# Kernel optimization log

Measured on AMD Instinct MI355X. Metric: run time of the kernel, lower is better.

## Reference

```python
import jax, jax.numpy as jnp
import numpy as np

B, L, DI = 256, 64, 2048   # batch, image regions, image feature dim
T, DT = 32, 512            # caption length, text embedding dim
U, A = 512, 512            # GRU units, attention units


def setup_inputs() -> dict:
    key = jax.random.key(0)
    ks = jax.random.split(key, 14)
    s = 0.02
    return {
        "img": jax.random.normal(ks[0], (B, L, DI), jnp.float32),
        "text": jax.random.normal(ks[1], (B, T, DT), jnp.float32),
        "kernel": jax.random.normal(ks[2], (DI + DT, 3 * U), jnp.float32) * s,
        "input_bias": jax.random.normal(ks[3], (3 * U,), jnp.float32) * s,
        "recurrent_kernel": jax.random.normal(ks[4], (U, 3 * U), jnp.float32) * s,
        "recurrent_bias": jax.random.normal(ks[5], (3 * U,), jnp.float32) * s,
        "att_img_kernel": jax.random.normal(ks[6], (DI, A), jnp.float32) * s,
        "att_img_bias": jax.random.normal(ks[7], (A,), jnp.float32) * s,
        "att_hidden_kernel": jax.random.normal(ks[8], (U, A), jnp.float32) * s,
        "att_hidden_bias": jax.random.normal(ks[9], (A,), jnp.float32) * s,
        "att_v_kernel": jax.random.normal(ks[10], (A, 1), jnp.float32) * s,
        "att_v_bias": jax.random.normal(ks[11], (1,), jnp.float32) * s,
    }


def reference(img, text, kernel, input_bias, recurrent_kernel, recurrent_bias,
              att_img_kernel, att_img_bias, att_hidden_kernel, att_hidden_bias,
              att_v_kernel, att_v_bias):
    # Precompute the image attention projection (independent of h; the
    # original recomputes it each step, but the math is identical).
    img_proj = jnp.einsum('bld,da->bla', img, att_img_kernel) + att_img_bias  # [B,L,A]

    def step(h, x_t):
        # Bahdanau attention over image regions
        hid = jnp.tanh(img_proj + (h @ att_hidden_kernel + att_hidden_bias)[:, None, :])  # [B,L,A]
        score = hid @ att_v_kernel + att_v_bias                # [B,L,1]
        attw = jax.nn.softmax(score, axis=1)                   # softmax over regions
        ctx = jnp.sum(attw * img, axis=1)                      # [B,DI]
        # GRU gate math (keras GRU v2 convention, reset gate applied after matmul)
        inp = jnp.concatenate([x_t, ctx], axis=-1)             # [B,DT+DI]
        mx = inp @ kernel + input_bias                         # [B,3U]
        mi = h @ recurrent_kernel + recurrent_bias             # [B,3U]
        x_z, x_r, x_h = jnp.split(mx, 3, axis=-1)
        r_z, r_r, r_h = jnp.split(mi, 3, axis=-1)
        z = jax.nn.sigmoid(x_z + r_z)
        r = jax.nn.sigmoid(x_r + r_r)
        hh = jnp.tanh(x_h + r * r_h)
        h_new = z * h + (1.0 - z) * hh
        return h_new, h_new

    h0 = jnp.zeros((img.shape[0], recurrent_kernel.shape[0]), img.dtype)
    _, seq = jax.lax.scan(step, h0, jnp.swapaxes(text, 0, 1))  # seq: [T,B,U]
    return jnp.swapaxes(seq, 0, 1)                             # [B,T,U]
```

## Files before the change

kernel.cpp:

```cpp
#include <hip/hip_runtime.h>
#include <hip/hip_bf16.h>

#define B_  256
#define L_  64
#define DI_ 2048
#define T_  32
#define DT_ 512
#define U_  512
#define A_  512
#define N3U 1536

typedef short short8 __attribute__((ext_vector_type(8)));
typedef float floatx4 __attribute__((ext_vector_type(4)));

__device__ __forceinline__ unsigned short f2bf(float f) {
  unsigned int u = __float_as_uint(f);
  u += 0x7fffu + ((u >> 16) & 1u);
  return (unsigned short)(u >> 16);
}
__device__ __forceinline__ float bf2f(unsigned short s) {
  return __uint_as_float(((unsigned int)s) << 16);
}
__device__ __forceinline__ float fast_tanh(float x) {
  x = fminf(fmaxf(x, -15.f), 15.f);
  float e = __expf(2.f * x);
  return (e - 1.f) / (e + 1.f);
}

__global__ __launch_bounds__(256) void gemm_a32_bt16_mfma(
    const float* __restrict__ A, const unsigned short* __restrict__ Bt,
    const float* __restrict__ bias, void* __restrict__ Cout,
    int M, int N, int K, int out_bf16) {
  __shared__ unsigned short As[128][40];
  __shared__ unsigned short Bs[128][40];
  const int tid  = threadIdx.x;
  const int wave = tid >> 6;
  const int lane = tid & 63;
  const int quad = lane >> 4;
  const int lr   = lane & 15;
  const int wrow = (wave >> 1) * 64;
  const int wcol = (wave & 1) * 64;
  const size_t bm = (size_t)blockIdx.y * 128;
  const size_t bn = (size_t)blockIdx.x * 128;

  const int sr = tid >> 2;
  const int sc = (tid & 3) * 8;

  floatx4 acc[4][4] = {};

  for (int k0 = 0; k0 < K; k0 += 32) {
#pragma unroll
    for (int it = 0; it < 2; ++it) {
      const int row = sr + it * 64;
      const float* ap = A + (bm + row) * (size_t)K + k0 + sc;
      float4 a0 = *(const float4*)(ap);
      float4 a1 = *(const float4*)(ap + 4);
      short8 pk;
      pk[0] = (short)f2bf(a0.x); pk[1] = (short)f2bf(a0.y);
      pk[2] = (short)f2bf(a0.z); pk[3] = (short)f2bf(a0.w);
      pk[4] = (short)f2bf(a1.x); pk[5] = (short)f2bf(a1.y);
      pk[6] = (short)f2bf(a1.z); pk[7] = (short)f2bf(a1.w);
      *(short8*)&As[row][sc] = pk;
      *(float4*)&Bs[row][sc] = *(const float4*)(Bt + (bn + row) * (size_t)K + k0 + sc);
    }
    __syncthreads();
    short8 af[4], bf[4];
#pragma unroll
    for (int mi = 0; mi < 4; ++mi) af[mi] = *(const short8*)&As[wrow + mi * 16 + lr][quad * 8];
#pragma unroll
    for (int ni = 0; ni < 4; ++ni) bf[ni] = *(const short8*)&Bs[wcol + ni * 16 + lr][quad * 8];
#pragma unroll
    for (int mi = 0; mi < 4; ++mi)
#pragma unroll
      for (int ni = 0; ni < 4; ++ni)
        acc[mi][ni] = __builtin_amdgcn_mfma_f32_16x16x32_bf16(af[mi], bf[ni], acc[mi][ni], 0, 0, 0);
    __syncthreads();
  }

  float* outf = (float*)Cout;
  unsigned short* outb = (unsigned short*)Cout;
#pragma unroll
  for (int mi = 0; mi < 4; ++mi) {
#pragma unroll
    for (int ni = 0; ni < 4; ++ni) {
      const size_t row0 = bm + wrow + mi * 16 + quad * 4;
      const size_t col  = bn + wcol + ni * 16 + lr;
      const float bsum = bias ? bias[col] : 0.f;
#pragma unroll
      for (int reg = 0; reg < 4; ++reg) {
        const float v = acc[mi][ni][reg] + bsum;
        if (out_bf16) outb[(row0 + reg) * (size_t)N + col] = f2bf(v);
        else          outf[(row0 + reg) * (size_t)N + col] = v;
      }
    }
  }
}

__global__ void zero_f32(float* __restrict__ p, int n) {
  int i = blockIdx.x * 256 + threadIdx.x;
  if (i < n) p[i] = 0.f;
}

__global__ __launch_bounds__(256) void transpose_f32_bf16(
    const float* __restrict__ in, unsigned short* __restrict__ outp, int K, int N) {
  __shared__ unsigned short tile[32][33];
  const int tid = threadIdx.x;
  const int tx = tid & 31, ty = tid >> 5;
  const int k0 = blockIdx.y * 32, n0 = blockIdx.x * 32;
#pragma unroll
  for (int i = 0; i < 4; ++i) {
    const int kk = ty + i * 8;
    tile[tx][kk] = f2bf(in[(size_t)(k0 + kk) * N + n0 + tx]);
  }
  __syncthreads();
#pragma unroll
  for (int i = 0; i < 4; ++i) {
    const int nn = ty + i * 8;
    outp[(size_t)(n0 + nn) * K + k0 + tx] = tile[nn][tx];
  }
}

__global__ void build_bcat(const float* __restrict__ ahb,
                           const float* __restrict__ rb,
                           float* __restrict__ bcat) {
  int i = blockIdx.x * 256 + threadIdx.x;
  if (i < A_) bcat[i] = ahb[i];
  else if (i < A_ + N3U) bcat[i] = rb[i - A_];
}

__global__ __launch_bounds__(512) void attn_gru_step(
    const unsigned short* __restrict__ img_proj,
    const unsigned short* __restrict__ imgW,
    const float* __restrict__ text_proj,
    const float* __restrict__ hm,
    const float* __restrict__ vk,
    float* __restrict__ h,
    float* __restrict__ out,
    int t) {
  const int b = blockIdx.x;
  const int tid = threadIdx.x;
  const int lane = tid & 63;
  const int wave = tid >> 6;
  __shared__ float sc[L_];
  __shared__ float aw[L_];

  const float* hpg = hm + (size_t)b * 2048;
  float hpv[8], vvv[8];
  {
    float4 h0 = *(const float4*)(hpg + lane * 8);
    float4 h1 = *(const float4*)(hpg + lane * 8 + 4);
    float4 v0 = *(const float4*)(vk + lane * 8);
    float4 v1 = *(const float4*)(vk + lane * 8 + 4);
    hpv[0]=h0.x; hpv[1]=h0.y; hpv[2]=h0.z; hpv[3]=h0.w;
    hpv[4]=h1.x; hpv[5]=h1.y; hpv[6]=h1.z; hpv[7]=h1.w;
    vvv[0]=v0.x; vvv[1]=v0.y; vvv[2]=v0.z; vvv[3]=v0.w;
    vvv[4]=v1.x; vvv[5]=v1.y; vvv[6]=v1.z; vvv[7]=v1.w;
  }

#pragma unroll
  for (int i = 0; i < 8; ++i) {
    const int l = wave + i * 8;
    const unsigned short* ip = img_proj + ((size_t)b * L_ + l) * A_ + lane * 8;
    short8 v8 = *(const short8*)ip;
    float s = 0.f;
#pragma unroll
    for (int j = 0; j < 8; ++j) {
      s += fast_tanh(bf2f((unsigned short)v8[j]) + hpv[j]) * vvv[j];
    }
#pragma unroll
    for (int off = 32; off; off >>= 1) s += __shfl_down(s, off);
    if (lane == 0) sc[l] = s;
  }
  __syncthreads();

  if (tid < 64) {
    float x = sc[tid];
    float m = x;
#pragma unroll
    for (int off = 32; off; off >>= 1) m = fmaxf(m, __shfl_xor(m, off));
    float e = __expf(x - m);
    float ssum = e;
#pragma unroll
    for (int off = 32; off; off >>= 1) ssum += __shfl_xor(ssum, off);
    aw[tid] = e / ssum;
  }
  __syncthreads();

  const int u = tid;
  const unsigned short* iw = imgW + (size_t)b * L_ * N3U + u;
  float s0 = 0.f, s1 = 0.f, s2 = 0.f;
#pragma unroll 8
  for (int l = 0; l < L_; ++l) {
    const float a = aw[l];
    const unsigned short* p = iw + l * N3U;
    s0 += a * bf2f(p[0]);
    s1 += a * bf2f(p[512]);
    s2 += a * bf2f(p[1024]);
  }
  const float* tp  = text_proj + ((size_t)b * T_ + t) * N3U;
  const float* mib = hm + (size_t)b * 2048 + 512;
  const float xz = s0 + tp[u]        + mib[u];
  const float xr = s1 + tp[512 + u]  + mib[512 + u];
  const float xh = s2 + tp[1024 + u];
  const float rh = mib[1024 + u];
  const float z = 1.f / (1.f + __expf(-xz));
  const float r = 1.f / (1.f + __expf(-xr));
  const float hh = fast_tanh(xh + r * rh);
  const float hn = z * h[b * U_ + u] + (1.f - z) * hh;
  h[b * U_ + u] = hn;
  out[((size_t)b * T_ + t) * U_ + u] = hn;
}

extern "C" void kernel_launch(void* const* d_in, const int* in_sizes, int n_in,
                              void* d_out, int out_size, void* d_ws, size_t ws_size,
                              hipStream_t stream) {
  const float* img        = (const float*)d_in[0];
  const float* text       = (const float*)d_in[1];
  const float* kern       = (const float*)d_in[2];
  const float* input_bias = (const float*)d_in[3];
  const float* rec_kern   = (const float*)d_in[4];
  const float* rec_bias   = (const float*)d_in[5];
  const float* att_img_k  = (const float*)d_in[6];
  const float* att_img_b  = (const float*)d_in[7];
  const float* att_hid_k  = (const float*)d_in[8];
  const float* att_hid_b  = (const float*)d_in[9];
  const float* att_v_k    = (const float*)d_in[10];
  float* out = (float*)d_out;

  char* ws = (char*)d_ws;
  size_t off = 0;
  auto alloc = [&](size_t bytes) { char* p = ws + off; off += (bytes + 255) & ~(size_t)255; return p; };
  unsigned short* img_proj = (unsigned short*)alloc((size_t)B_*L_*A_*2);
  unsigned short* imgW     = (unsigned short*)alloc((size_t)B_*L_*N3U*2);
  float*          text_proj= (float*)         alloc((size_t)B_*T_*N3U*4);
  unsigned short* wt1      = (unsigned short*)alloc((size_t)A_*DI_*2);
  unsigned short* wt2      = (unsigned short*)alloc((size_t)N3U*DI_*2);
  unsigned short* wt3      = (unsigned short*)alloc((size_t)N3U*DT_*2);
  unsigned short* wcatT    = (unsigned short*)alloc((size_t)2048*U_*2);
  float*          bcat     = (float*)         alloc(2048*4);
  float*          h        = (float*)         alloc((size_t)B_*U_*4);
  float*          hm       = (float*)         alloc((size_t)B_*2048*4);

  dim3 blk(256);

  zero_f32<<<dim3((B_*U_ + 255) / 256), blk, 0, stream>>>(h, B_*U_);

  transpose_f32_bf16<<<dim3(A_/32, DI_/32), blk, 0, stream>>>(att_img_k, wt1, DI_, A_);
  transpose_f32_bf16<<<dim3(N3U/32, DI_/32), blk, 0, stream>>>(kern + (size_t)DT_*N3U, wt2, DI_, N3U);
  transpose_f32_bf16<<<dim3(N3U/32, DT_/32), blk, 0, stream>>>(kern, wt3, DT_, N3U);
  transpose_f32_bf16<<<dim3(A_/32, U_/32), blk, 0, stream>>>(att_hid_k, wcatT, U_, A_);
  transpose_f32_bf16<<<dim3(N3U/32, U_/32), blk, 0, stream>>>(rec_kern, wcatT + (size_t)A_*U_, U_, N3U);
  build_bcat<<<dim3(8), blk, 0, stream>>>(att_hid_b, rec_bias, bcat);

  gemm_a32_bt16_mfma<<<dim3(A_/128, (B_*L_)/128), blk, 0, stream>>>(
      img, wt1, att_img_b, img_proj, B_*L_, A_, DI_, 1);
  gemm_a32_bt16_mfma<<<dim3(N3U/128, (B_*L_)/128), blk, 0, stream>>>(
      img, wt2, nullptr, imgW, B_*L_, N3U, DI_, 1);
  gemm_a32_bt16_mfma<<<dim3(N3U/128, (B_*T_)/128), blk, 0, stream>>>(
      text, wt3, input_bias, text_proj, B_*T_, N3U, DT_, 0);

  for (int t = 0; t < T_; ++t) {
    gemm_a32_bt16_mfma<<<dim3(2048/128, B_/128), blk, 0, stream>>>(
        h, wcatT, bcat, hm, B_, 2048, U_, 0);
    attn_gru_step<<<dim3(B_), dim3(512), 0, stream>>>(
        img_proj, imgW, text_proj, hm, att_v_k, h, out, t);
  }
}
```

Measured before the change: 1.765 ms.

## Fuse recurrent loop into single cooperative kernel with grid syncs

Result: slower. 3.473 ms (+96.7%).

```diff
diff --git a/kernel.cpp b/kernel.cpp
--- a/kernel.cpp
+++ b/kernel.cpp
@@ -1,5 +1,8 @@
 #include <hip/hip_runtime.h>
 #include <hip/hip_bf16.h>
+#include <hip/hip_cooperative_groups.h>
+
+namespace cg = cooperative_groups;
 
 #define B_  256
 #define L_  64
@@ -25,6 +28,9 @@
   x = fminf(fmaxf(x, -15.f), 15.f);
   float e = __expf(2.f * x);
   return (e - 1.f) / (e + 1.f);
+}
+__device__ __forceinline__ float sigmoidf(float x) {
+  return 1.f / (1.f + __expf(-x));
 }
 
 __global__ __launch_bounds__(256) void gemm_a32_bt16_mfma(
@@ -96,11 +102,6 @@
   }
 }
 
-__global__ void zero_f32(float* __restrict__ p, int n) {
-  int i = blockIdx.x * 256 + threadIdx.x;
-  if (i < n) p[i] = 0.f;
-}
-
 __global__ __launch_bounds__(256) void transpose_f32_bf16(
     const float* __restrict__ in, unsigned short* __restrict__ outp, int K, int N) {
   __shared__ unsigned short tile[32][33];
@@ -128,87 +129,130 @@
   else if (i < A_ + N3U) bcat[i] = rb[i - A_];
 }
 
-__global__ __launch_bounds__(512) void attn_gru_step(
+__global__ __launch_bounds__(512) void recurrence_coop(
     const unsigned short* __restrict__ img_proj,
     const unsigned short* __restrict__ imgW,
     const float* __restrict__ text_proj,
-    const float* __restrict__ hm,
+    const unsigned short* __restrict__ wcatT,
+    const float* __restrict__ bcat,
     const float* __restrict__ vk,
     float* __restrict__ h,
-    float* __restrict__ out,
-    int t) {
-  const int b = blockIdx.x;
-  const int tid = threadIdx.x;
+    unsigned short* __restrict__ hbf,
+    float* __restrict__ hm,
+    float* __restrict__ out) {
+  cg::grid_group grid = cg::this_grid();
+  const int bid  = blockIdx.x;
+  const int tid  = threadIdx.x;
   const int lane = tid & 63;
   const int wave = tid >> 6;
+  const int quad = lane >> 4;
+  const int lr   = lane & 15;
+
   __shared__ float sc[L_];
   __shared__ float aw[L_];
-
-  const float* hpg = hm + (size_t)b * 2048;
-  float hpv[8], vvv[8];
+  __shared__ float mxs[N3U];
+
+  h[bid * U_ + tid] = 0.f;
+  hbf[bid * U_ + tid] = 0;
+  grid.sync();
+
+  const int n0  = (bid >> 1) * 16;
+  const int m0w = (bid & 1) * 128 + wave * 16;
+  const float bsum = bcat[n0 + lr];
+
+  float vvv[8];
   {
-    float4 h0 = *(const float4*)(hpg + lane * 8);
-    float4 h1 = *(const float4*)(hpg + lane * 8 + 4);
     float4 v0 = *(const float4*)(vk + lane * 8);
     float4 v1 = *(const float4*)(vk + lane * 8 + 4);
-    hpv[0]=h0.x; hpv[1]=h0.y; hpv[2]=h0.z; hpv[3]=h0.w;
-    hpv[4]=h1.x; hpv[5]=h1.y; hpv[6]=h1.z; hpv[7]=h1.w;
     vvv[0]=v0.x; vvv[1]=v0.y; vvv[2]=v0.z; vvv[3]=v0.w;
     vvv[4]=v1.x; vvv[5]=v1.y; vvv[6]=v1.z; vvv[7]=v1.w;
   }
 
-#pragma unroll
-  for (int i = 0; i < 8; ++i) {
-    const int l = wave + i * 8;
-    const unsigned short* ip = img_proj + ((size_t)b * L_ + l) * A_ + lane * 8;
-    short8 v8 = *(const short8*)ip;
-    float s = 0.f;
-#pragma unroll
-    for (int j = 0; j < 8; ++j) {
-      s += fast_tanh(bf2f((unsigned short)v8[j]) + hpv[j]) * vvv[j];
-    }
-#pragma unroll
-    for (int off = 32; off; off >>= 1) s += __shfl_down(s, off);
-    if (lane == 0) sc[l] = s;
-  }
-  __syncthreads();
-
-  if (tid < 64) {
-    float x = sc[tid];
-    float m = x;
-#pragma unroll
-    for (int off = 32; off; off >>= 1) m = fmaxf(m, __shfl_xor(m, off));
-    float e = __expf(x - m);
-    float ssum = e;
-#pragma unroll
-    for (int off = 32; off; off >>= 1) ssum += __shfl_xor(ssum, off);
-    aw[tid] = e / ssum;
-  }
-  __syncthreads();
-
-  const int u = tid;
-  const unsigned short* iw = imgW + (size_t)b * L_ * N3U + u;
-  float s0 = 0.f, s1 = 0.f, s2 = 0.f;
-#pragma unroll 8
-  for (int l = 0; l < L_; ++l) {
-    const float a = aw[l];
-    const unsigned short* p = iw + l * N3U;
-    s0 += a * bf2f(p[0]);
-    s1 += a * bf2f(p[512]);
-    s2 += a * bf2f(p[1024]);
-  }
-  const float* tp  = text_proj + ((size_t)b * T_ + t) * N3U;
-  const float* mib = hm + (size_t)b * 2048 + 512;
-  const float xz = s0 + tp[u]        + mib[u];
-  const float xr = s1 + tp[512 + u]  + mib[512 + u];
-  const float xh = s2 + tp[1024 + u];
-  const float rh = mib[1024 + u];
-  const float z = 1.f / (1.f + __expf(-xz));
-  const float r = 1.f / (1.f + __expf(-xr));
-  const float hh = fast_tanh(xh + r * rh);
-  const float hn = z * h[b * U_ + u] + (1.f - z) * hh;
-  h[b * U_ + u] = hn;
-  out[((size_t)b * T_ + t) * U_ + u] = hn;
+  for (int t = 0; t < T_; ++t) {
+    {
+      floatx4 acc = {0.f, 0.f, 0.f, 0.f};
+      const unsigned short* ab = hbf + (size_t)(m0w + lr) * U_;
+      const unsigned short* bb = wcatT + (size_t)(n0 + lr) * U_;
+#pragma unroll
+      for (int k0 = 0; k0 < U_; k0 += 32) {
+        short8 afr = *(const short8*)(ab + k0 + quad * 8);
+        short8 bfr = *(const short8*)(bb + k0 + quad * 8);
+        acc = __builtin_amdgcn_mfma_f32_16x16x32_bf16(afr, bfr, acc, 0, 0, 0);
+      }
+#pragma unroll
+      for (int r = 0; r < 4; ++r)
+        hm[(size_t)(m0w + quad * 4 + r) * 2048 + n0 + lr] = acc[r] + bsum;
+    }
+    grid.sync();
+
+    {
+      const float* hp = hm + (size_t)bid * 2048;
+      float hpv[8];
+      float4 h0 = *(const float4*)(hp + lane * 8);
+      float4 h1 = *(const float4*)(hp + lane * 8 + 4);
+      hpv[0]=h0.x; hpv[1]=h0.y; hpv[2]=h0.z; hpv[3]=h0.w;
+      hpv[4]=h1.x; hpv[5]=h1.y; hpv[6]=h1.z; hpv[7]=h1.w;
+#pragma unroll
+      for (int i = 0; i < 8; ++i) {
+        const int l = wave + i * 8;
+        short8 v8 = *(const short8*)(img_proj + ((size_t)bid * L_ + l) * A_ + lane * 8);
+        float s = 0.f;
+#pragma unroll
+        for (int j = 0; j < 8; ++j)
+          s += fast_tanh(bf2f((unsigned short)v8[j]) + hpv[j]) * vvv[j];
+#pragma unroll
+        for (int off = 32; off; off >>= 1) s += __shfl_down(s, off);
+        if (lane == 0) sc[l] = s;
+      }
+      __syncthreads();
+      if (tid < 64) {
+        float x = sc[tid];
+        float m = x;
+#pragma unroll
+        for (int off = 32; off; off >>= 1) m = fmaxf(m, __shfl_xor(m, off));
+        float e = __expf(x - m);
+        float ssum = e;
+#pragma unroll
+        for (int off = 32; off; off >>= 1) ssum += __shfl_xor(ssum, off);
+        aw[tid] = e / ssum;
+      }
+      __syncthreads();
+    }
+
+    if (tid < 384) {
+      const unsigned short* iwp = imgW + (size_t)bid * L_ * N3U + tid * 4;
+      float a0 = 0.f, a1 = 0.f, a2 = 0.f, a3 = 0.f;
+#pragma unroll 16
+      for (int l = 0; l < L_; ++l) {
+        const float a = aw[l];
+        ushort4 w = *(const ushort4*)(iwp + (size_t)l * N3U);
+        a0 += a * bf2f(w.x); a1 += a * bf2f(w.y);
+        a2 += a * bf2f(w.z); a3 += a * bf2f(w.w);
+      }
+      float4 t4 = *(const float4*)(text_proj + ((size_t)bid * T_ + t) * N3U + tid * 4);
+      mxs[tid * 4 + 0] = a0 + t4.x;
+      mxs[tid * 4 + 1] = a1 + t4.y;
+      mxs[tid * 4 + 2] = a2 + t4.z;
+      mxs[tid * 4 + 3] = a3 + t4.w;
+    }
+    __syncthreads();
+    {
+      const int u = tid;
+      const float* mib = hm + (size_t)bid * 2048 + 512;
+      const float xz = mxs[u]        + mib[u];
+      const float xr = mxs[512 + u]  + mib[512 + u];
+      const float xh = mxs[1024 + u];
+      const float rh = mib[1024 + u];
+      const float z = sigmoidf(xz);
+      const float r = sigmoidf(xr);
+      const float hh = fast_tanh(xh + r * rh);
+      const float hn = z * h[bid * U_ + u] + (1.f - z) * hh;
+      h[bid * U_ + u] = hn;
+      hbf[bid * U_ + u] = f2bf(hn);
+      out[((size_t)bid * T_ + t) * U_ + u] = hn;
+    }
+    grid.sync();
+  }
 }
 
 extern "C" void kernel_launch(void* const* d_in, const int* in_sizes, int n_in,
@@ -239,11 +283,10 @@
   unsigned short* wcatT    = (unsigned short*)alloc((size_t)2048*U_*2);
   float*          bcat     = (float*)         alloc(2048*4);
   float*          h        = (float*)         alloc((size_t)B_*U_*4);
+  unsigned short* hbf      = (unsigned short*)alloc((size_t)B_*U_*2);
   float*          hm       = (float*)         alloc((size_t)B_*2048*4);
 
   dim3 blk(256);
-
-  zero_f32<<<dim3((B_*U_ + 255) / 256), blk, 0, stream>>>(h, B_*U_);
 
   transpose_f32_bf16<<<dim3(A_/32, DI_/32), blk, 0, stream>>>(att_img_k, wt1, DI_, A_);
   transpose_f32_bf16<<<dim3(N3U/32, DI_/32), blk, 0, stream>>>(kern + (size_t)DT_*N3U, wt2, DI_, N3U);
@@ -259,10 +302,9 @@
   gemm_a32_bt16_mfma<<<dim3(N3U/128, (B_*T_)/128), blk, 0, stream>>>(
       text, wt3, input_bias, text_proj, B_*T_, N3U, DT_, 0);
 
-  for (int t = 0; t < T_; ++t) {
-    gemm_a32_bt16_mfma<<<dim3(2048/128, B_/128), blk, 0, stream>>>(
-        h, wcatT, bcat, hm, B_, 2048, U_, 0);
-    attn_gru_step<<<dim3(B_), dim3(512), 0, stream>>>(
-        img_proj, imgW, text_proj, hm, att_v_k, h, out, t);
-  }
-}
+  void* args[] = { (void*)&img_proj, (void*)&imgW, (void*)&text_proj,
+                   (void*)&wcatT, (void*)&bcat, (void*)&att_v_k,
+                   (void*)&h, (void*)&hbf, (void*)&hm, (void*)&out };
+  hipLaunchCooperativeKernel((const void*)recurrence_coop,
+                             dim3(B_), dim3(512), args, 0, stream);
+}
```
